# Optimization experiments

Hardware: AMD Instinct MI355X
Metric: run time of the kernel (lower is better)

The kernel has to match this reference:

```python
import jax, jax.numpy as jnp
import numpy as np

B, N, D, L = 32, 1024, 128, 2  # batch graphs, nodes, hidden dim, num GIN layers
BN_EPS = 1e-5


def _batchnorm(x2d, gamma, beta):
    # Training-mode BatchNorm1d over flattened (B*N, D) with biased variance
    mean = jnp.mean(x2d, axis=0)
    var = jnp.mean(jnp.square(x2d - mean), axis=0)
    return (x2d - mean) * (gamma / jnp.sqrt(var + BN_EPS)) + beta


def setup_inputs() -> dict:
    key = jax.random.key(0)
    ks = jax.random.split(key, 12)
    s = 1.0 / np.sqrt(D)  # torch Linear default init scale
    inp = {
        "x": jax.random.normal(ks[0], (B, N, D), dtype=jnp.float32),
        "padded_nei": jax.random.randint(ks[1], (B, N, 8), 0, N, dtype=jnp.int64),
        "adj": jax.random.uniform(ks[2], (B, N, N), dtype=jnp.float32),
        # stacked per-layer params [L, ...]
        "W1": jax.random.uniform(ks[3], (L, D, D), jnp.float32, -s, s),
        "b1": jax.random.uniform(ks[4], (L, D), jnp.float32, -s, s),
        "W2": jax.random.uniform(ks[5], (L, D, D), jnp.float32, -s, s),
        "b2": jax.random.uniform(ks[6], (L, D), jnp.float32, -s, s),
        "g_in": jnp.ones((L, D), jnp.float32),   # MLP-internal BN gamma
        "be_in": jnp.zeros((L, D), jnp.float32),  # MLP-internal BN beta
        "g_out": jnp.ones((L, D), jnp.float32),  # GraphCNN outer BN gamma
        "be_out": jnp.zeros((L, D), jnp.float32),
    }
    return inp


def reference(x, padded_nei, adj, W1, b1, W2, b2, g_in, be_in, g_out, be_out):
    h = x  # [B, N, D]
    for l in range(L):
        # sum-pooling over neighbors via batched dense adjacency matmul
        pooled = jnp.einsum('bij,bjd->bid', adj, h)  # [B, N, D]
        # MLP: Linear -> BN -> ReLU -> Linear
        z = pooled @ W1[l] + b1[l]
        z = jax.nn.relu(_batchnorm(z.reshape(-1, D), g_in[l], be_in[l])).reshape(B, N, D)
        z = z @ W2[l] + b2[l]
        # outer BatchNorm1d + ReLU
        h = jax.nn.relu(_batchnorm(z.reshape(-1, D), g_out[l], be_out[l])).reshape(B, N, D)
    return h
```

## Files before the change

### kernel.cpp

```cpp
#include <hip/hip_runtime.h>
#include <stdint.h>


#define BB 32
#define NN 1024
#define DD 128
#define RR 32768

typedef __bf16 bf16_t;
typedef bf16_t bf16x8 __attribute__((ext_vector_type(8)));
typedef float f32x4 __attribute__((ext_vector_type(4)));

__device__ __forceinline__ unsigned short f2b(float f) {
  unsigned u = __float_as_uint(f);
  u += 0x7fff + ((u >> 16) & 1);
  return (unsigned short)(u >> 16);
}

__global__ __launch_bounds__(256) void k0_xT(const float* __restrict__ x,
                                             unsigned short* __restrict__ hT) {
  const int b = blockIdx.x, nt = blockIdx.y, tid = threadIdx.x;
  __shared__ alignas(16) unsigned short T[128][136];
  const int r = tid >> 1, c0 = (tid & 1) * 64;
  const float* src = x + ((size_t)(b * 8 + nt) * 128 + r) * 128 + c0;
#pragma unroll
  for (int i = 0; i < 64; i += 4) {
    float4 v = *(const float4*)(src + i);
    int c = c0 + i;
    T[c][r] = f2b(v.x); T[c + 1][r] = f2b(v.y);
    T[c + 2][r] = f2b(v.z); T[c + 3][r] = f2b(v.w);
  }
  __syncthreads();
  const int d = tid >> 1, n0 = (tid & 1) * 64;
  unsigned short* dst = hT + ((size_t)b * DD + d) * NN + nt * 128 + n0;
#pragma unroll
  for (int i = 0; i < 64; i += 8)
    *(uint4*)(dst + i) = *(const uint4*)&T[d][n0 + i];
}

__global__ __launch_bounds__(256) void k0_wT(const float* __restrict__ W1,
                                             const float* __restrict__ W2,
                                             unsigned short* __restrict__ W1T,
                                             unsigned short* __restrict__ W2T) {
  int idx = blockIdx.x * 256 + threadIdx.x;
  int w = idx >> 15;
  int rem = idx & 32767;
  int l = rem >> 14;
  int n = (rem >> 7) & 127;
  int k = rem & 127;
  const float* W = w ? W2 : W1;
  unsigned short* WT = w ? W2T : W1T;
  WT[((size_t)l * 128 + n) * 128 + k] = f2b(W[((size_t)l * 128 + k) * 128 + n]);
}

__global__ __launch_bounds__(256) void k1_pool(const float* __restrict__ adj,
                                               const unsigned short* __restrict__ hT,
                                               unsigned short* __restrict__ pooled) {
  const int mt = blockIdx.x, b = blockIdx.y;
  const int tid = threadIdx.x;
  const int wave = tid >> 6, lane = tid & 63;
  const int wr = (wave >> 1) * 64, wc = (wave & 1) * 64;
  const int ln = lane & 15, q = lane >> 4;

  __shared__ alignas(16) unsigned short As[128][40];
  __shared__ alignas(16) unsigned short Bs[128][40];

  const float* adjb = adj + ((size_t)b * NN + mt * 128) * NN;
  const unsigned short* hTb = hT + (size_t)b * DD * NN;

  f32x4 acc[4][4];
  f32x4 zero = {0.f, 0.f, 0.f, 0.f};
#pragma unroll
  for (int i = 0; i < 4; i++)
#pragma unroll
    for (int j = 0; j < 4; j++) acc[i][j] = zero;

  const int rs = tid >> 1;
  const int hs = tid & 1;

  for (int k0 = 0; k0 < NN; k0 += 32) {
    __syncthreads();
    {
      const float* src = adjb + (size_t)rs * NN + k0 + hs * 16;
      alignas(16) unsigned short t[16];
#pragma unroll
      for (int i = 0; i < 16; i += 4) {
        float4 v = *(const float4*)(src + i);
        t[i] = f2b(v.x); t[i + 1] = f2b(v.y); t[i + 2] = f2b(v.z); t[i + 3] = f2b(v.w);
      }
      *(uint4*)&As[rs][hs * 16] = *(const uint4*)&t[0];
      *(uint4*)&As[rs][hs * 16 + 8] = *(const uint4*)&t[8];
    }
    {
      const unsigned short* src = hTb + (size_t)rs * NN + k0 + hs * 16;
      *(uint4*)&Bs[rs][hs * 16] = *(const uint4*)(src);
      *(uint4*)&Bs[rs][hs * 16 + 8] = *(const uint4*)(src + 8);
    }
    __syncthreads();
    bf16x8 af[4], bfr[4];
#pragma unroll
    for (int i = 0; i < 4; i++) af[i] = *(const bf16x8*)&As[wr + i * 16 + ln][q * 8];
#pragma unroll
    for (int j = 0; j < 4; j++) bfr[j] = *(const bf16x8*)&Bs[wc + j * 16 + ln][q * 8];
#pragma unroll
    for (int i = 0; i < 4; i++)
#pragma unroll
      for (int j = 0; j < 4; j++)
        acc[i][j] = __builtin_amdgcn_mfma_f32_16x16x32_bf16(af[i], bfr[j], acc[i][j], 0, 0, 0);
  }

  unsigned short* outb = pooled + ((size_t)b * NN + mt * 128) * DD;
#pragma unroll
  for (int i = 0; i < 4; i++) {
    int row = wr + i * 16 + q * 4;
#pragma unroll
    for (int j = 0; j < 4; j++) {
      int col = wc + j * 16 + ln;
#pragma unroll
      for (int r = 0; r < 4; r++)
        outb[(size_t)(row + r) * DD + col] = f2b(acc[i][j][r]);
    }
  }
}

__global__ __launch_bounds__(256) void k2_lin(const unsigned short* __restrict__ Ain,
                                              const unsigned short* __restrict__ WT,
                                              const float* __restrict__ bias,
                                              float* __restrict__ Z,
                                              float* __restrict__ gsum,
                                              float* __restrict__ gsq) {
  const int mt = blockIdx.x;
  const int tid = threadIdx.x;
  const int wave = tid >> 6, lane = tid & 63;
  const int wr = (wave >> 1) * 64, wc = (wave & 1) * 64;
  const int ln = lane & 15, q = lane >> 4;

  __shared__ alignas(16) unsigned short As[128][40];
  __shared__ alignas(16) unsigned short Ws[128][136];
  __shared__ float lsum[128], lsq[128];

  if (tid < 128) { lsum[tid] = 0.f; lsq[tid] = 0.f; }
#pragma unroll
  for (int p = 0; p < 8; p++) {
    int c = tid + p * 256;
    int n = c >> 4, k8 = (c & 15) * 8;
    *(uint4*)&Ws[n][k8] = *(const uint4*)&WT[n * 128 + k8];
  }

  f32x4 acc[4][4];
  f32x4 zero = {0.f, 0.f, 0.f, 0.f};
#pragma unroll
  for (int i = 0; i < 4; i++)
#pragma unroll
    for (int j = 0; j < 4; j++) acc[i][j] = zero;

  const int rs = tid >> 1, hs = tid & 1;
  const size_t row0 = (size_t)mt * 128;

  for (int k0 = 0; k0 < 128; k0 += 32) {
    __syncthreads();
    const unsigned short* src = Ain + (row0 + rs) * 128 + k0 + hs * 16;
    *(uint4*)&As[rs][hs * 16] = *(const uint4*)src;
    *(uint4*)&As[rs][hs * 16 + 8] = *(const uint4*)(src + 8);
    __syncthreads();
    bf16x8 af[4], bfr[4];
#pragma unroll
    for (int i = 0; i < 4; i++) af[i] = *(const bf16x8*)&As[wr + i * 16 + ln][q * 8];
#pragma unroll
    for (int j = 0; j < 4; j++) bfr[j] = *(const bf16x8*)&Ws[wc + j * 16 + ln][k0 + q * 8];
#pragma unroll
    for (int i = 0; i < 4; i++)
#pragma unroll
      for (int j = 0; j < 4; j++)
        acc[i][j] = __builtin_amdgcn_mfma_f32_16x16x32_bf16(af[i], bfr[j], acc[i][j], 0, 0, 0);
  }

  float s1[4] = {0.f, 0.f, 0.f, 0.f}, s2[4] = {0.f, 0.f, 0.f, 0.f};
  float* Zb = Z + row0 * 128;
#pragma unroll
  for (int j = 0; j < 4; j++) {
    int col = wc + j * 16 + ln;
    float bc = bias[col];
#pragma unroll
    for (int i = 0; i < 4; i++) {
      int row = wr + i * 16 + q * 4;
#pragma unroll
      for (int r = 0; r < 4; r++) {
        float v = acc[i][j][r] + bc;
        Zb[(size_t)(row + r) * 128 + col] = v;
        s1[j] += v; s2[j] += v * v;
      }
    }
  }
#pragma unroll
  for (int j = 0; j < 4; j++) {
    s1[j] += __shfl_xor(s1[j], 16); s1[j] += __shfl_xor(s1[j], 32);
    s2[j] += __shfl_xor(s2[j], 16); s2[j] += __shfl_xor(s2[j], 32);
  }
  if (q == 0) {
#pragma unroll
    for (int j = 0; j < 4; j++) {
      atomicAdd(&lsum[wc + j * 16 + ln], s1[j]);
      atomicAdd(&lsq[wc + j * 16 + ln], s2[j]);
    }
  }
  __syncthreads();
  if (tid < 128) atomicAdd(&gsum[tid], lsum[tid]);
  else atomicAdd(&gsq[tid - 128], lsq[tid - 128]);
}

__global__ __launch_bounds__(256) void k3_lin(const float* __restrict__ Zin,
                                              const float* __restrict__ gsum_in,
                                              const float* __restrict__ gsq_in,
                                              const float* __restrict__ gamma,
                                              const float* __restrict__ beta,
                                              const unsigned short* __restrict__ WT,
                                              const float* __restrict__ bias,
                                              float* __restrict__ Z,
                                              float* __restrict__ gsum,
                                              float* __restrict__ gsq) {
  const int mt = blockIdx.x;
  const int tid = threadIdx.x;
  const int wave = tid >> 6, lane = tid & 63;
  const int wr = (wave >> 1) * 64, wc = (wave & 1) * 64;
  const int ln = lane & 15, q = lane >> 4;

  __shared__ alignas(16) unsigned short As[128][40];
  __shared__ alignas(16) unsigned short Ws[128][136];
  __shared__ float lsum[128], lsq[128];
  __shared__ float nsc[128], nsh[128];

  if (tid < 128) {
    float mean = gsum_in[tid] * (1.f / 32768.f);
    float var = gsq_in[tid] * (1.f / 32768.f) - mean * mean;
    float sc = gamma[tid] * rsqrtf(var + 1e-5f);
    nsc[tid] = sc; nsh[tid] = beta[tid] - mean * sc;
    lsum[tid] = 0.f; lsq[tid] = 0.f;
  }
#pragma unroll
  for (int p = 0; p < 8; p++) {
    int c = tid + p * 256;
    int n = c >> 4, k8 = (c & 15) * 8;
    *(uint4*)&Ws[n][k8] = *(const uint4*)&WT[n * 128 + k8];
  }

  f32x4 acc[4][4];
  f32x4 zero = {0.f, 0.f, 0.f, 0.f};
#pragma unroll
  for (int i = 0; i < 4; i++)
#pragma unroll
    for (int j = 0; j < 4; j++) acc[i][j] = zero;

  const int rs = tid >> 1, hs = tid & 1;
  const size_t row0 = (size_t)mt * 128;

  for (int k0 = 0; k0 < 128; k0 += 32) {
    __syncthreads();
    {
      const float* src = Zin + (row0 + rs) * 128 + k0 + hs * 16;
      alignas(16) unsigned short t[16];
#pragma unroll
      for (int i = 0; i < 16; i += 4) {
        float4 v = *(const float4*)(src + i);
        int c = k0 + hs * 16 + i;
        t[i]     = f2b(fmaxf(fmaf(v.x, nsc[c], nsh[c]), 0.f));
        t[i + 1] = f2b(fmaxf(fmaf(v.y, nsc[c + 1], nsh[c + 1]), 0.f));
        t[i + 2] = f2b(fmaxf(fmaf(v.z, nsc[c + 2], nsh[c + 2]), 0.f));
        t[i + 3] = f2b(fmaxf(fmaf(v.w, nsc[c + 3], nsh[c + 3]), 0.f));
      }
      *(uint4*)&As[rs][hs * 16] = *(const uint4*)&t[0];
      *(uint4*)&As[rs][hs * 16 + 8] = *(const uint4*)&t[8];
    }
    __syncthreads();
    bf16x8 af[4], bfr[4];
#pragma unroll
    for (int i = 0; i < 4; i++) af[i] = *(const bf16x8*)&As[wr + i * 16 + ln][q * 8];
#pragma unroll
    for (int j = 0; j < 4; j++) bfr[j] = *(const bf16x8*)&Ws[wc + j * 16 + ln][k0 + q * 8];
#pragma unroll
    for (int i = 0; i < 4; i++)
#pragma unroll
      for (int j = 0; j < 4; j++)
        acc[i][j] = __builtin_amdgcn_mfma_f32_16x16x32_bf16(af[i], bfr[j], acc[i][j], 0, 0, 0);
  }

  float s1[4] = {0.f, 0.f, 0.f, 0.f}, s2[4] = {0.f, 0.f, 0.f, 0.f};
  float* Zb = Z + row0 * 128;
#pragma unroll
  for (int j = 0; j < 4; j++) {
    int col = wc + j * 16 + ln;
    float bc = bias[col];
#pragma unroll
    for (int i = 0; i < 4; i++) {
      int row = wr + i * 16 + q * 4;
#pragma unroll
      for (int r = 0; r < 4; r++) {
        float v = acc[i][j][r] + bc;
        Zb[(size_t)(row + r) * 128 + col] = v;
        s1[j] += v; s2[j] += v * v;
      }
    }
  }
#pragma unroll
  for (int j = 0; j < 4; j++) {
    s1[j] += __shfl_xor(s1[j], 16); s1[j] += __shfl_xor(s1[j], 32);
    s2[j] += __shfl_xor(s2[j], 16); s2[j] += __shfl_xor(s2[j], 32);
  }
  if (q == 0) {
#pragma unroll
    for (int j = 0; j < 4; j++) {
      atomicAdd(&lsum[wc + j * 16 + ln], s1[j]);
      atomicAdd(&lsq[wc + j * 16 + ln], s2[j]);
    }
  }
  __syncthreads();
  if (tid < 128) atomicAdd(&gsum[tid], lsum[tid]);
  else atomicAdd(&gsq[tid - 128], lsq[tid - 128]);
}

__global__ __launch_bounds__(256) void k4_bnt(const float* __restrict__ Z,
                                              const float* __restrict__ gsum,
                                              const float* __restrict__ gsq,
                                              const float* __restrict__ gamma,
                                              const float* __restrict__ beta,
                                              unsigned short* __restrict__ hT) {
  const int b = blockIdx.x, nt = blockIdx.y, tid = threadIdx.x;
  __shared__ alignas(16) unsigned short T[128][136];
  __shared__ float nsc[128], nsh[128];
  if (tid < 128) {
    float mean = gsum[tid] * (1.f / 32768.f);
    float var = gsq[tid] * (1.f / 32768.f) - mean * mean;
    float sc = gamma[tid] * rsqrtf(var + 1e-5f);
    nsc[tid] = sc; nsh[tid] = beta[tid] - mean * sc;
  }
  __syncthreads();
  const int r = tid >> 1, c0 = (tid & 1) * 64;
  const float* src = Z + ((size_t)(b * 8 + nt) * 128 + r) * 128 + c0;
#pragma unroll
  for (int i = 0; i < 64; i += 4) {
    float4 v = *(const float4*)(src + i);
    int c = c0 + i;
    T[c][r]     = f2b(fmaxf(fmaf(v.x, nsc[c], nsh[c]), 0.f));
    T[c + 1][r] = f2b(fmaxf(fmaf(v.y, nsc[c + 1], nsh[c + 1]), 0.f));
    T[c + 2][r] = f2b(fmaxf(fmaf(v.z, nsc[c + 2], nsh[c + 2]), 0.f));
    T[c + 3][r] = f2b(fmaxf(fmaf(v.w, nsc[c + 3], nsh[c + 3]), 0.f));
  }
  __syncthreads();
  const int d = tid >> 1, n0 = (tid & 1) * 64;
  unsigned short* dst = hT + ((size_t)b * DD + d) * NN + nt * 128 + n0;
#pragma unroll
  for (int i = 0; i < 64; i += 8)
    *(uint4*)(dst + i) = *(const uint4*)&T[d][n0 + i];
}

__global__ __launch_bounds__(256) void k4_out(const float* __restrict__ Z,
                                              const float* __restrict__ gsum,
                                              const float* __restrict__ gsq,
                                              const float* __restrict__ gamma,
                                              const float* __restrict__ beta,
                                              float* __restrict__ out) {
  const int blk = blockIdx.x, tid = threadIdx.x;
  __shared__ float nsc[128], nsh[128];
  if (tid < 128) {
    float mean = gsum[tid] * (1.f / 32768.f);
    float var = gsq[tid] * (1.f / 32768.f) - mean * mean;
    float sc = gamma[tid] * rsqrtf(var + 1e-5f);
    nsc[tid] = sc; nsh[tid] = beta[tid] - mean * sc;
  }
  __syncthreads();
  const int r = tid >> 1, c0 = (tid & 1) * 64;
  const float* src = Z + ((size_t)blk * 128 + r) * 128 + c0;
  float* dst = out + ((size_t)blk * 128 + r) * 128 + c0;
#pragma unroll
  for (int i = 0; i < 64; i += 4) {
    float4 v = *(const float4*)(src + i);
    int c = c0 + i;
    float4 o;
    o.x = fmaxf(fmaf(v.x, nsc[c], nsh[c]), 0.f);
    o.y = fmaxf(fmaf(v.y, nsc[c + 1], nsh[c + 1]), 0.f);
    o.z = fmaxf(fmaf(v.z, nsc[c + 2], nsh[c + 2]), 0.f);
    o.w = fmaxf(fmaf(v.w, nsc[c + 3], nsh[c + 3]), 0.f);
    *(float4*)(dst + i) = o;
  }
}

extern "C" void kernel_launch(void* const* d_in, const int* in_sizes, int n_in,
                              void* d_out, int out_size, void* d_ws, size_t ws_size,
                              hipStream_t stream) {
  const float* x = (const float*)d_in[0];
  const float* adj = (const float*)d_in[2];
  const float* W1 = (const float*)d_in[3];
  const float* b1 = (const float*)d_in[4];
  const float* W2 = (const float*)d_in[5];
  const float* b2 = (const float*)d_in[6];
  const float* g_in = (const float*)d_in[7];
  const float* be_in = (const float*)d_in[8];
  const float* g_out = (const float*)d_in[9];
  const float* be_out = (const float*)d_in[10];
  float* out = (float*)d_out;

  char* ws = (char*)d_ws;
  unsigned short* hT = (unsigned short*)ws;
  float* z1 = (float*)(ws + 8ull * 1024 * 1024);
  float* z2 = (float*)(ws + 24ull * 1024 * 1024);
  unsigned short* pooled = (unsigned short*)(ws + 24ull * 1024 * 1024);
  unsigned short* W1T = (unsigned short*)(ws + 40ull * 1024 * 1024);
  unsigned short* W2T = W1T + 2 * 128 * 128;
  float* stats = (float*)(ws + 40ull * 1024 * 1024 + 256 * 1024);

  hipMemsetAsync(stats, 0, 4 * 256 * sizeof(float), stream);

  k0_xT<<<dim3(32, 8), 256, 0, stream>>>(x, hT);
  k0_wT<<<256, 256, 0, stream>>>(W1, W2, W1T, W2T);

  for (int l = 0; l < 2; l++) {
    float* st_in = stats + (l * 2 + 0) * 256;
    float* st_out = stats + (l * 2 + 1) * 256;
    k1_pool<<<dim3(8, 32), 256, 0, stream>>>(adj, hT, pooled);
    k2_lin<<<256, 256, 0, stream>>>(pooled, W1T + l * 16384, b1 + l * 128, z1,
                                    st_in, st_in + 128);
    k3_lin<<<256, 256, 0, stream>>>(z1, st_in, st_in + 128, g_in + l * 128,
                                    be_in + l * 128, W2T + l * 16384, b2 + l * 128,
                                    z2, st_out, st_out + 128);
    if (l == 0)
      k4_bnt<<<dim3(32, 8), 256, 0, stream>>>(z2, st_out, st_out + 128, g_out,
                                              be_out, hT);
    else
      k4_out<<<256, 256, 0, stream>>>(z2, st_out, st_out + 128, g_out + 128,
                                      be_out + 128, out);
  }
}
```

Measured before the change: 379.0 us.

## Fuse pooling with first linear, store intermediates in bf16, prefetch adj tiles

Merges the adjacency pooling GEMM and the first Linear into one kernel that keeps the pooled tile in shared memory, so the pooled buffer never goes to global memory. Z1 and Z2 are now stored as bf16 instead of fp32, halving intermediate traffic. The pooling loop uses a 64-row M tile, a 64-wide K step, and register prefetch of the next adj/hT slice. Stats reductions go straight to global atomics, and the two prep kernels are merged into one launch. Extra bf16 rounding of pre-BN activations may reduce accuracy, and the smaller M tile rereads hT more often.

```diff
diff --git a/kernel.cpp b/kernel.cpp
--- a/kernel.cpp
+++ b/kernel.cpp
@@ -16,130 +16,68 @@
   u += 0x7fff + ((u >> 16) & 1);
   return (unsigned short)(u >> 16);
 }
-
-__global__ __launch_bounds__(256) void k0_xT(const float* __restrict__ x,
-                                             unsigned short* __restrict__ hT) {
-  const int b = blockIdx.x, nt = blockIdx.y, tid = threadIdx.x;
-  __shared__ alignas(16) unsigned short T[128][136];
-  const int r = tid >> 1, c0 = (tid & 1) * 64;
-  const float* src = x + ((size_t)(b * 8 + nt) * 128 + r) * 128 + c0;
-#pragma unroll
-  for (int i = 0; i < 64; i += 4) {
-    float4 v = *(const float4*)(src + i);
-    int c = c0 + i;
-    T[c][r] = f2b(v.x); T[c + 1][r] = f2b(v.y);
-    T[c + 2][r] = f2b(v.z); T[c + 3][r] = f2b(v.w);
-  }
-  __syncthreads();
-  const int d = tid >> 1, n0 = (tid & 1) * 64;
-  unsigned short* dst = hT + ((size_t)b * DD + d) * NN + nt * 128 + n0;
-#pragma unroll
-  for (int i = 0; i < 64; i += 8)
-    *(uint4*)(dst + i) = *(const uint4*)&T[d][n0 + i];
-}
-
-__global__ __launch_bounds__(256) void k0_wT(const float* __restrict__ W1,
-                                             const float* __restrict__ W2,
-                                             unsigned short* __restrict__ W1T,
-                                             unsigned short* __restrict__ W2T) {
-  int idx = blockIdx.x * 256 + threadIdx.x;
-  int w = idx >> 15;
-  int rem = idx & 32767;
-  int l = rem >> 14;
-  int n = (rem >> 7) & 127;
-  int k = rem & 127;
-  const float* W = w ? W2 : W1;
-  unsigned short* WT = w ? W2T : W1T;
-  WT[((size_t)l * 128 + n) * 128 + k] = f2b(W[((size_t)l * 128 + k) * 128 + n]);
-}
-
-__global__ __launch_bounds__(256) void k1_pool(const float* __restrict__ adj,
-                                               const unsigned short* __restrict__ hT,
-                                               unsigned short* __restrict__ pooled) {
+__device__ __forceinline__ float b2f(unsigned short s) {
+  return __uint_as_float((unsigned)s << 16);
+}
+
+__global__ __launch_bounds__(256) void k0_prep(const float* __restrict__ x,
+                                               const float* __restrict__ W1,
+                                               const float* __restrict__ W2,
+                                               unsigned short* __restrict__ hT,
+                                               unsigned short* __restrict__ W1T,
+                                               unsigned short* __restrict__ W2T) {
+  const int tid = threadIdx.x;
+  if (blockIdx.x < 256) {
+    const int b = blockIdx.x >> 3, nt = blockIdx.x & 7;
+    __shared__ alignas(16) unsigned short T[128][136];
+    const int r = tid >> 1, c0 = (tid & 1) * 64;
+    const float* src = x + ((size_t)(b * 8 + nt) * 128 + r) * 128 + c0;
+#pragma unroll
+    for (int i = 0; i < 64; i += 4) {
+      float4 v = *(const float4*)(src + i);
+      int c = c0 + i;
+      T[c][r] = f2b(v.x); T[c + 1][r] = f2b(v.y);
+      T[c + 2][r] = f2b(v.z); T[c + 3][r] = f2b(v.w);
+    }
+    __syncthreads();
+    const int d = tid >> 1, n0 = (tid & 1) * 64;
+    unsigned short* dst = hT + ((size_t)b * DD + d) * NN + nt * 128 + n0;
+#pragma unroll
+    for (int i = 0; i < 64; i += 8)
+      *(uint4*)(dst + i) = *(const uint4*)&T[d][n0 + i];
+  } else {
+    int idx = (blockIdx.x - 256) * 256 + tid;
+    int w = idx >> 15;
+    int rem = idx & 32767;
+    int l = rem >> 14;
+    int n = (rem >> 7) & 127;
+    int k = rem & 127;
+    const float* W = w ? W2 : W1;
+    unsigned short* WT = w ? W2T : W1T;
+    WT[((size_t)l * 128 + n) * 128 + k] = f2b(W[((size_t)l * 128 + k) * 128 + n]);
+  }
+}
+
+__global__ __launch_bounds__(256, 2) void kA_pool_lin(
+    const float* __restrict__ adj, const unsigned short* __restrict__ hT,
+    const unsigned short* __restrict__ WT, const float* __restrict__ bias,
+    unsigned short* __restrict__ z1b, float* __restrict__ gsum,
+    float* __restrict__ gsq) {
   const int mt = blockIdx.x, b = blockIdx.y;
   const int tid = threadIdx.x;
   const int wave = tid >> 6, lane = tid & 63;
-  const int wr = (wave >> 1) * 64, wc = (wave & 1) * 64;
+  const int wc = wave * 32;
   const int ln = lane & 15, q = lane >> 4;
 
-  __shared__ alignas(16) unsigned short As[128][40];
-  __shared__ alignas(16) unsigned short Bs[128][40];
-
-  const float* adjb = adj + ((size_t)b * NN + mt * 128) * NN;
-  const unsigned short* hTb = hT + (size_t)b * DD * NN;
-
-  f32x4 acc[4][4];
-  f32x4 zero = {0.f, 0.f, 0.f, 0.f};
-#pragma unroll
-  for (int i = 0; i < 4; i++)
-#pragma unroll
-    for (int j = 0; j < 4; j++) acc[i][j] = zero;
-
-  const int rs = tid >> 1;
-  const int hs = tid & 1;
-
-  for (int k0 = 0; k0 < NN; k0 += 32) {
-    __syncthreads();
-    {
-      const float* src = adjb + (size_t)rs * NN + k0 + hs * 16;
-      alignas(16) unsigned short t[16];
-#pragma unroll
-      for (int i = 0; i < 16; i += 4) {
-        float4 v = *(const float4*)(src + i);
-        t[i] = f2b(v.x); t[i + 1] = f2b(v.y); t[i + 2] = f2b(v.z); t[i + 3] = f2b(v.w);
-      }
-      *(uint4*)&As[rs][hs * 16] = *(const uint4*)&t[0];
-      *(uint4*)&As[rs][hs * 16 + 8] = *(const uint4*)&t[8];
-    }
-    {
-      const unsigned short* src = hTb + (size_t)rs * NN + k0 + hs * 16;
-      *(uint4*)&Bs[rs][hs * 16] = *(const uint4*)(src);
-      *(uint4*)&Bs[rs][hs * 16 + 8] = *(const uint4*)(src + 8);
-    }
-    __syncthreads();
-    bf16x8 af[4], bfr[4];
-#pragma unroll
-    for (int i = 0; i < 4; i++) af[i] = *(const bf16x8*)&As[wr + i * 16 + ln][q * 8];
-#pragma unroll
-    for (int j = 0; j < 4; j++) bfr[j] = *(const bf16x8*)&Bs[wc + j * 16 + ln][q * 8];
-#pragma unroll
-    for (int i = 0; i < 4; i++)
-#pragma unroll
-      for (int j = 0; j < 4; j++)
-        acc[i][j] = __builtin_amdgcn_mfma_f32_16x16x32_bf16(af[i], bfr[j], acc[i][j], 0, 0, 0);
-  }
-
-  unsigned short* outb = pooled + ((size_t)b * NN + mt * 128) * DD;
-#pragma unroll
-  for (int i = 0; i < 4; i++) {
-    int row = wr + i * 16 + q * 4;
-#pragma unroll
-    for (int j = 0; j < 4; j++) {
-      int col = wc + j * 16 + ln;
-#pragma unroll
-      for (int r = 0; r < 4; r++)
-        outb[(size_t)(row + r) * DD + col] = f2b(acc[i][j][r]);
-    }
-  }
-}
-
-__global__ __launch_bounds__(256) void k2_lin(const unsigned short* __restrict__ Ain,
-                                              const unsigned short* __restrict__ WT,
-                                              const float* __restrict__ bias,
-                                              float* __restrict__ Z,
-                                              float* __restrict__ gsum,
-                                              float* __restrict__ gsq) {
-  const int mt = blockIdx.x;
-  const int tid = threadIdx.x;
-  const int wave = tid >> 6, lane = tid & 63;
-  const int wr = (wave >> 1) * 64, wc = (wave & 1) * 64;
-  const int ln = lane & 15, q = lane >> 4;
-
-  __shared__ alignas(16) unsigned short As[128][40];
+  __shared__ union {
+    struct {
+      alignas(16) unsigned short As[64][72];
+      alignas(16) unsigned short Bs[128][72];
+    } p1;
+    alignas(16) unsigned short As2[64][136];
+  } sm;
   __shared__ alignas(16) unsigned short Ws[128][136];
-  __shared__ float lsum[128], lsq[128];
-
-  if (tid < 128) { lsum[tid] = 0.f; lsq[tid] = 0.f; }
+
 #pragma unroll
   for (int p = 0; p < 8; p++) {
     int c = tid + p * 256;
@@ -147,87 +85,134 @@
     *(uint4*)&Ws[n][k8] = *(const uint4*)&WT[n * 128 + k8];
   }
 
-  f32x4 acc[4][4];
+  const float* adjb = adj + ((size_t)b * NN + mt * 64) * NN;
+  const unsigned short* hTb = hT + (size_t)b * DD * NN;
+
+  f32x4 acc1[4][2];
   f32x4 zero = {0.f, 0.f, 0.f, 0.f};
 #pragma unroll
-  for (int i = 0; i < 4; i++)
-#pragma unroll
-    for (int j = 0; j < 4; j++) acc[i][j] = zero;
-
-  const int rs = tid >> 1, hs = tid & 1;
-  const size_t row0 = (size_t)mt * 128;
-
-  for (int k0 = 0; k0 < 128; k0 += 32) {
+  for (int i = 0; i < 4; i++) { acc1[i][0] = zero; acc1[i][1] = zero; }
+
+  const int ar = tid >> 2, aseg = (tid & 3) * 16;
+  const int br = tid >> 1, bh = (tid & 1) * 32;
+  const float* pAsrc = adjb + (size_t)ar * NN + aseg;
+  const unsigned short* pBsrc = hTb + (size_t)br * NN + bh;
+
+  float4 pa[4];
+  uint4 pb[4];
+#pragma unroll
+  for (int u = 0; u < 4; u++) {
+    pa[u] = *(const float4*)(pAsrc + u * 4);
+    pb[u] = *(const uint4*)(pBsrc + u * 8);
+  }
+
+  for (int k0 = 0; k0 < NN; k0 += 64) {
     __syncthreads();
-    const unsigned short* src = Ain + (row0 + rs) * 128 + k0 + hs * 16;
-    *(uint4*)&As[rs][hs * 16] = *(const uint4*)src;
-    *(uint4*)&As[rs][hs * 16 + 8] = *(const uint4*)(src + 8);
+    {
+      alignas(16) unsigned short t[16];
+#pragma unroll
+      for (int u = 0; u < 4; u++) {
+        t[u * 4] = f2b(pa[u].x); t[u * 4 + 1] = f2b(pa[u].y);
+        t[u * 4 + 2] = f2b(pa[u].z); t[u * 4 + 3] = f2b(pa[u].w);
+      }
+      *(uint4*)&sm.p1.As[ar][aseg] = *(const uint4*)&t[0];
+      *(uint4*)&sm.p1.As[ar][aseg + 8] = *(const uint4*)&t[8];
+#pragma unroll
+      for (int u = 0; u < 4; u++) *(uint4*)&sm.p1.Bs[br][bh + u * 8] = pb[u];
+    }
     __syncthreads();
-    bf16x8 af[4], bfr[4];
-#pragma unroll
-    for (int i = 0; i < 4; i++) af[i] = *(const bf16x8*)&As[wr + i * 16 + ln][q * 8];
-#pragma unroll
-    for (int j = 0; j < 4; j++) bfr[j] = *(const bf16x8*)&Ws[wc + j * 16 + ln][k0 + q * 8];
+    if (k0 + 64 < NN) {
+#pragma unroll
+      for (int u = 0; u < 4; u++) {
+        pa[u] = *(const float4*)(pAsrc + k0 + 64 + u * 4);
+        pb[u] = *(const uint4*)(pBsrc + k0 + 64 + u * 8);
+      }
+    }
+#pragma unroll
+    for (int kk = 0; kk < 2; kk++) {
+      bf16x8 af[4], bfr[2];
+#pragma unroll
+      for (int i = 0; i < 4; i++)
+        af[i] = *(const bf16x8*)&sm.p1.As[i * 16 + ln][kk * 32 + q * 8];
+#pragma unroll
+      for (int j = 0; j < 2; j++)
+        bfr[j] = *(const bf16x8*)&sm.p1.Bs[wc + j * 16 + ln][kk * 32 + q * 8];
+#pragma unroll
+      for (int i = 0; i < 4; i++)
+#pragma unroll
+        for (int j = 0; j < 2; j++)
+          acc1[i][j] = __builtin_amdgcn_mfma_f32_16x16x32_bf16(af[i], bfr[j], acc1[i][j], 0, 0, 0);
+    }
+  }
+
+  __syncthreads();
+#pragma unroll
+  for (int i = 0; i < 4; i++) {
+    int row = i * 16 + q * 4;
+#pragma unroll
+    for (int j = 0; j < 2; j++) {
+      int col = wc + j * 16 + ln;
+#pragma unroll
+      for (int r = 0; r < 4; r++) sm.As2[row + r][col] = f2b(acc1[i][j][r]);
+    }
+  }
+  __syncthreads();
+
+  f32x4 acc2[4][2];
+#pragma unroll
+  for (int i = 0; i < 4; i++) { acc2[i][0] = zero; acc2[i][1] = zero; }
+#pragma unroll
+  for (int ks = 0; ks < 4; ks++) {
+    bf16x8 af[4], bfr[2];
 #pragma unroll
     for (int i = 0; i < 4; i++)
-#pragma unroll
-      for (int j = 0; j < 4; j++)
-        acc[i][j] = __builtin_amdgcn_mfma_f32_16x16x32_bf16(af[i], bfr[j], acc[i][j], 0, 0, 0);
-  }
-
-  float s1[4] = {0.f, 0.f, 0.f, 0.f}, s2[4] = {0.f, 0.f, 0.f, 0.f};
-  float* Zb = Z + row0 * 128;
-#pragma unroll
-  for (int j = 0; j < 4; j++) {
+      af[i] = *(const bf16x8*)&sm.As2[i * 16 + ln][ks * 32 + q * 8];
+#pragma unroll
+    for (int j = 0; j < 2; j++)
+      bfr[j] = *(const bf16x8*)&Ws[wc + j * 16 + ln][ks * 32 + q * 8];
+#pragma unroll
+    for (int i = 0; i < 4; i++)
+#pragma unroll
+      for (int j = 0; j < 2; j++)
+        acc2[i][j] = __builtin_amdgcn_mfma_f32_16x16x32_bf16(af[i], bfr[j], acc2[i][j], 0, 0, 0);
+  }
+
+  const size_t row0 = (size_t)b * NN + mt * 64;
+#pragma unroll
+  for (int j = 0; j < 2; j++) {
     int col = wc + j * 16 + ln;
     float bc = bias[col];
+    float s1 = 0.f, s2 = 0.f;
 #pragma unroll
     for (int i = 0; i < 4; i++) {
-      int row = wr + i * 16 + q * 4;
+      int row = i * 16 + q * 4;
 #pragma unroll
       for (int r = 0; r < 4; r++) {
-        float v = acc[i][j][r] + bc;
-        Zb[(size_t)(row + r) * 128 + col] = v;
-        s1[j] += v; s2[j] += v * v;
+        float v = acc2[i][j][r] + bc;
+        z1b[(row0 + row + r) * 128 + col] = f2b(v);
+        s1 += v; s2 += v * v;
       }
     }
-  }
-#pragma unroll
-  for (int j = 0; j < 4; j++) {
-    s1[j] += __shfl_xor(s1[j], 16); s1[j] += __shfl_xor(s1[j], 32);
-    s2[j] += __shfl_xor(s2[j], 16); s2[j] += __shfl_xor(s2[j], 32);
-  }
-  if (q == 0) {
-#pragma unroll
-    for (int j = 0; j < 4; j++) {
-      atomicAdd(&lsum[wc + j * 16 + ln], s1[j]);
-      atomicAdd(&lsq[wc + j * 16 + ln], s2[j]);
-    }
-  }
-  __syncthreads();
-  if (tid < 128) atomicAdd(&gsum[tid], lsum[tid]);
-  else atomicAdd(&gsq[tid - 128], lsq[tid - 128]);
-}
-
-__global__ __launch_bounds__(256) void k3_lin(const float* __restrict__ Zin,
-                                              const float* __restrict__ gsum_in,
-                                              const float* __restrict__ gsq_in,
-                                              const float* __restrict__ gamma,
-                                              const float* __restrict__ beta,
-                                              const unsigned short* __restrict__ WT,
-                                              const float* __restrict__ bias,
-                                              float* __restrict__ Z,
-                                              float* __restrict__ gsum,
-                                              float* __restrict__ gsq) {
+    s1 += __shfl_xor(s1, 16); s1 += __shfl_xor(s1, 32);
+    s2 += __shfl_xor(s2, 16); s2 += __shfl_xor(s2, 32);
+    if (q == 0) { atomicAdd(&gsum[col], s1); atomicAdd(&gsq[col], s2); }
+  }
+}
+
+__global__ __launch_bounds__(256, 2) void kB_lin(
+    const unsigned short* __restrict__ Zin, const float* __restrict__ gsum_in,
+    const float* __restrict__ gsq_in, const float* __restrict__ gamma,
+    const float* __restrict__ beta, const unsigned short* __restrict__ WT,
+    const float* __restrict__ bias, unsigned short* __restrict__ z2b,
+    float* __restrict__ gsum, float* __restrict__ gsq) {
   const int mt = blockIdx.x;
   const int tid = threadIdx.x;
   const int wave = tid >> 6, lane = tid & 63;
-  const int wr = (wave >> 1) * 64, wc = (wave & 1) * 64;
+  const int wc = wave * 32;
   const int ln = lane & 15, q = lane >> 4;
 
-  __shared__ alignas(16) unsigned short As[128][40];
+  __shared__ alignas(16) unsigned short Az[64][136];
   __shared__ alignas(16) unsigned short Ws[128][136];
-  __shared__ float lsum[128], lsq[128];
   __shared__ float nsc[128], nsh[128];
 
   if (tid < 128) {
@@ -235,7 +220,6 @@
     float var = gsq_in[tid] * (1.f / 32768.f) - mean * mean;
     float sc = gamma[tid] * rsqrtf(var + 1e-5f);
     nsc[tid] = sc; nsh[tid] = beta[tid] - mean * sc;
-    lsum[tid] = 0.f; lsq[tid] = 0.f;
   }
 #pragma unroll
   for (int p = 0; p < 8; p++) {
@@ -243,82 +227,69 @@
     int n = c >> 4, k8 = (c & 15) * 8;
     *(uint4*)&Ws[n][k8] = *(const uint4*)&WT[n * 128 + k8];
   }
-
-  f32x4 acc[4][4];
+  __syncthreads();
+
+  const size_t row0 = (size_t)mt * 64;
+  {
+    const int r = tid >> 2, c0 = (tid & 3) * 32;
+    const unsigned short* src = Zin + (row0 + r) * 128 + c0;
+#pragma unroll
+    for (int u = 0; u < 4; u++) {
+      uint4 raw = *(const uint4*)(src + u * 8);
+      const unsigned short* s = (const unsigned short*)&raw;
+      alignas(16) unsigned short t[8];
+#pragma unroll
+      for (int e = 0; e < 8; e++) {
+        int c = c0 + u * 8 + e;
+        t[e] = f2b(fmaxf(fmaf(b2f(s[e]), nsc[c], nsh[c]), 0.f));
+      }
+      *(uint4*)&Az[r][c0 + u * 8] = *(const uint4*)&t[0];
+    }
+  }
+  __syncthreads();
+
+  f32x4 acc[4][2];
   f32x4 zero = {0.f, 0.f, 0.f, 0.f};
 #pragma unroll
-  for (int i = 0; i < 4; i++)
-#pragma unroll
-    for (int j = 0; j < 4; j++) acc[i][j] = zero;
-
-  const int rs = tid >> 1, hs = tid & 1;
-  const size_t row0 = (size_t)mt * 128;
-
-  for (int k0 = 0; k0 < 128; k0 += 32) {
-    __syncthreads();
-    {
-      const float* src = Zin + (row0 + rs) * 128 + k0 + hs * 16;
-      alignas(16) unsigned short t[16];
-#pragma unroll
-      for (int i = 0; i < 16; i += 4) {
-        float4 v = *(const float4*)(src + i);
-        int c = k0 + hs * 16 + i;
-        t[i]     = f2b(fmaxf(fmaf(v.x, nsc[c], nsh[c]), 0.f));
-        t[i + 1] = f2b(fmaxf(fmaf(v.y, nsc[c + 1], nsh[c + 1]), 0.f));
-        t[i + 2] = f2b(fmaxf(fmaf(v.z, nsc[c + 2], nsh[c + 2]), 0.f));
-        t[i + 3] = f2b(fmaxf(fmaf(v.w, nsc[c + 3], nsh[c + 3]), 0.f));
-      }
-      *(uint4*)&As[rs][hs * 16] = *(const uint4*)&t[0];
-      *(uint4*)&As[rs][hs * 16 + 8] = *(const uint4*)&t[8];
-    }
-    __syncthreads();
-    bf16x8 af[4], bfr[4];
-#pragma unroll
-    for (int i = 0; i < 4; i++) af[i] = *(const bf16x8*)&As[wr + i * 16 + ln][q * 8];
-#pragma unroll
-    for (int j = 0; j < 4; j++) bfr[j] = *(const bf16x8*)&Ws[wc + j * 16 + ln][k0 + q * 8];
+  for (int i = 0; i < 4; i++) { acc[i][0] = zero; acc[i][1] = zero; }
+#pragma unroll
+  for (int ks = 0; ks < 4; ks++) {
+    bf16x8 af[4], bfr[2];
 #pragma unroll
     for (int i = 0; i < 4; i++)
-#pragma unroll
-      for (int j = 0; j < 4; j++)
+      af[i] = *(const bf16x8*)&Az[i * 16 + ln][ks * 32 + q * 8];
+#pragma unroll
+    for (int j = 0; j < 2; j++)
+      bfr[j] = *(const bf16x8*)&Ws[wc + j * 16 + ln][ks * 32 + q * 8];
+#pragma unroll
+    for (int i = 0; i < 4; i++)
+#pragma unroll
+      for (int j = 0; j < 2; j++)
         acc[i][j] = __builtin_amdgcn_mfma_f32_16x16x32_bf16(af[i], bfr[j], acc[i][j], 0, 0, 0);
   }
 
-  float s1[4] = {0.f, 0.f, 0.f, 0.f}, s2[4] = {0.f, 0.f, 0.f, 0.f};
-  float* Zb = Z + row0 * 128;
-#pragma unroll
-  for (int j = 0; j < 4; j++) {
+#pragma unroll
+  for (int j = 0; j < 2; j++) {
     int col = wc + j * 16 + ln;
     float bc = bias[col];
+    float s1 = 0.f, s2 = 0.f;
 #pragma unroll
     for (int i = 0; i < 4; i++) {
-      int row = wr + i * 16 + q * 4;
+      int row = i * 16 + q * 4;
 #pragma unroll
       for (int r = 0; r < 4; r++) {
         float v = acc[i][j][r] + bc;
-        Zb[(size_t)(row + r) * 128 + col] = v;
-        s1[j] += v; s2[j] += v * v;
+        z2b[(row0 + row + r) * 128 + col] = f2b(v);
+        s1 += v; s2 += v * v;
       }
     }
-  }
-#pragma unroll
-  for (int j = 0; j < 4; j++) {
-    s1[j] += __shfl_xor(s1[j], 16); s1[j] += __shfl_xor(s1[j], 32);
-    s2[j] += __shfl_xor(s2[j], 16); s2[j] += __shfl_xor(s2[j], 32);
-  }
-  if (q == 0) {
-#pragma unroll
-    for (int j = 0; j < 4; j++) {
-      atomicAdd(&lsum[wc + j * 16 + ln], s1[j]);
-      atomicAdd(&lsq[wc + j * 16 + ln], s2[j]);
-    }
-  }
-  __syncthreads();
-  if (tid < 128) atomicAdd(&gsum[tid], lsum[tid]);
-  else atomicAdd(&gsq[tid - 128], lsq[tid - 128]);
-}
-
-__global__ __launch_bounds__(256) void k4_bnt(const float* __restrict__ Z,
+    s1 += __shfl_xor(s1, 16); s1 += __shfl_xor(s1, 32);
+    s2 += __shfl_xor(s2, 16); s2 += __shfl_xor(s2, 32);
+    if (q == 0) { atomicAdd(&gsum[col], s1); atomicAdd(&gsq[col], s2); }
+  }
+}
+
+__global__ __launch_bounds__(256) void k4_bnt(const unsigned short* __restrict__ Z,
                                               const float* __restrict__ gsum,
                                               const float* __restrict__ gsq,
                                               const float* __restrict__ gamma,
@@ -335,15 +306,16 @@
   }
   __syncthreads();
   const int r = tid >> 1, c0 = (tid & 1) * 64;
-  const float* src = Z + ((size_t)(b * 8 + nt) * 128 + r) * 128 + c0;
-#pragma unroll
-  for (int i = 0; i < 64; i += 4) {
-    float4 v = *(const float4*)(src + i);
-    int c = c0 + i;
-    T[c][r]     = f2b(fmaxf(fmaf(v.x, nsc[c], nsh[c]), 0.f));
-    T[c + 1][r] = f2b(fmaxf(fmaf(v.y, nsc[c + 1], nsh[c + 1]), 0.f));
-    T[c + 2][r] = f2b(fmaxf(fmaf(v.z, nsc[c + 2], nsh[c + 2]), 0.f));
-    T[c + 3][r] = f2b(fmaxf(fmaf(v.w, nsc[c + 3], nsh[c + 3]), 0.f));
+  const unsigned short* src = Z + ((size_t)(b * 8 + nt) * 128 + r) * 128 + c0;
+#pragma unroll
+  for (int u = 0; u < 8; u++) {
+    uint4 raw = *(const uint4*)(src + u * 8);
+    const unsigned short* s = (const unsigned short*)&raw;
+#pragma unroll
+    for (int e = 0; e < 8; e++) {
+      int c = c0 + u * 8 + e;
+      T[c][r] = f2b(fmaxf(fmaf(b2f(s[e]), nsc[c], nsh[c]), 0.f));
+    }
   }
   __syncthreads();
   const int d = tid >> 1, n0 = (tid & 1) * 64;
@@ -353,7 +325,7 @@
     *(uint4*)(dst + i) = *(const uint4*)&T[d][n0 + i];
 }
 
-__global__ __launch_bounds__(256) void k4_out(const float* __restrict__ Z,
+__global__ __launch_bounds__(256) void k4_out(const unsigned short* __restrict__ Z,
                                               const float* __restrict__ gsum,
                                               const float* __restrict__ gsq,
                                               const float* __restrict__ gamma,
@@ -369,18 +341,24 @@
   }
   __syncthreads();
   const int r = tid >> 1, c0 = (tid & 1) * 64;
-  const float* src = Z + ((size_t)blk * 128 + r) * 128 + c0;
+  const unsigned short* src = Z + ((size_t)blk * 128 + r) * 128 + c0;
   float* dst = out + ((size_t)blk * 128 + r) * 128 + c0;
 #pragma unroll
-  for (int i = 0; i < 64; i += 4) {
-    float4 v = *(const float4*)(src + i);
-    int c = c0 + i;
+  for (int u = 0; u < 8; u++) {
+    uint4 raw = *(const uint4*)(src + u * 8);
+    const unsigned short* s = (const unsigned short*)&raw;
     float4 o;
-    o.x = fmaxf(fmaf(v.x, nsc[c], nsh[c]), 0.f);
-    o.y = fmaxf(fmaf(v.y, nsc[c + 1], nsh[c + 1]), 0.f);
-    o.z = fmaxf(fmaf(v.z, nsc[c + 2], nsh[c + 2]), 0.f);
-    o.w = fmaxf(fmaf(v.w, nsc[c + 3], nsh[c + 3]), 0.f);
-    *(float4*)(dst + i) = o;
+    int c = c0 + u * 8;
+    o.x = fmaxf(fmaf(b2f(s[0]), nsc[c], nsh[c]), 0.f);
+    o.y = fmaxf(fmaf(b2f(s[1]), nsc[c + 1], nsh[c + 1]), 0.f);
+    o.z = fmaxf(fmaf(b2f(s[2]), nsc[c + 2], nsh[c + 2]), 0.f);
+    o.w = fmaxf(fmaf(b2f(s[3]), nsc[c + 3], nsh[c + 3]), 0.f);
+    *(float4*)(dst + u * 8) = o;
+    o.x = fmaxf(fmaf(b2f(s[4]), nsc[c + 4], nsh[c + 4]), 0.f);
+    o.y = fmaxf(fmaf(b2f(s[5]), nsc[c + 5], nsh[c + 5]), 0.f);
+    o.z = fmaxf(fmaf(b2f(s[6]), nsc[c + 6], nsh[c + 6]), 0.f);
+    o.w = fmaxf(fmaf(b2f(s[7]), nsc[c + 7], nsh[c + 7]), 0.f);
+    *(float4*)(dst + u * 8 + 4) = o;
   }
 }
 
@@ -401,32 +379,29 @@
 
   char* ws = (char*)d_ws;
   unsigned short* hT = (unsigned short*)ws;
-  float* z1 = (float*)(ws + 8ull * 1024 * 1024);
-  float* z2 = (float*)(ws + 24ull * 1024 * 1024);
-  unsigned short* pooled = (unsigned short*)(ws + 24ull * 1024 * 1024);
-  unsigned short* W1T = (unsigned short*)(ws + 40ull * 1024 * 1024);
+  unsigned short* z1b = (unsigned short*)(ws + 8ull * 1024 * 1024);
+  unsigned short* z2b = (unsigned short*)(ws + 16ull * 1024 * 1024);
+  unsigned short* W1T = (unsigned short*)(ws + 24ull * 1024 * 1024);
   unsigned short* W2T = W1T + 2 * 128 * 128;
-  float* stats = (float*)(ws + 40ull * 1024 * 1024 + 256 * 1024);
+  float* stats = (float*)(ws + 25ull * 1024 * 1024);
 
   hipMemsetAsync(stats, 0, 4 * 256 * sizeof(float), stream);
-
-  k0_xT<<<dim3(32, 8), 256, 0, stream>>>(x, hT);
-  k0_wT<<<256, 256, 0, stream>>>(W1, W2, W1T, W2T);
+  k0_prep<<<512, 256, 0, stream>>>(x, W1, W2, hT, W1T, W2T);
 
   for (int l = 0; l < 2; l++) {
     float* st_in = stats + (l * 2 + 0) * 256;
     float* st_out = stats + (l * 2 + 1) * 256;
-    k1_pool<<<dim3(8, 32), 256, 0, stream>>>(adj, hT, pooled);
-    k2_lin<<<256, 256, 0, stream>>>(pooled, W1T + l * 16384, b1 + l * 128, z1,
-                                    st_in, st_in + 128);
-    k3_lin<<<256, 256, 0, stream>>>(z1, st_in, st_in + 128, g_in + l * 128,
-                                    be_in + l * 128, W2T + l * 16384, b2 + l * 128,
-                                    z2, st_out, st_out + 128);
+    kA_pool_lin<<<dim3(16, 32), 256, 0, stream>>>(adj, hT, W1T + l * 16384,
+                                                  b1 + l * 128, z1b, st_in,
+                                                  st_in + 128);
+    kB_lin<<<512, 256, 0, stream>>>(z1b, st_in, st_in + 128, g_in + l * 128,
+                                    be_in + l * 128, W2T + l * 16384,
+                                    b2 + l * 128, z2b, st_out, st_out + 128);
     if (l == 0)
-      k4_bnt<<<dim3(32, 8), 256, 0, stream>>>(z2, st_out, st_out + 128, g_out,
+      k4_bnt<<<dim3(32, 8), 256, 0, stream>>>(z2b, st_out, st_out + 128, g_out,
                                               be_out, hT);
     else
-      k4_out<<<256, 256, 0, stream>>>(z2, st_out, st_out + 128, g_out + 128,
+      k4_out<<<256, 256, 0, stream>>>(z2b, st_out, st_out + 128, g_out + 128,
                                       be_out + 128, out);
   }
 }
```

Measured after the change: 354.6 us. 1.07x faster.
